# Kernel tuning notes

Hardware: AMD Instinct MI355X
Metric: run time of the kernel (lower is better)

## Reference

```python
import jax, jax.numpy as jnp
import numpy as np

N, D, NUM_CLASSES = 4096, 1024, 64


def setup_inputs() -> dict:
    key = jax.random.key(0)
    k1, k2 = jax.random.split(key)
    inputs = jax.random.normal(k1, (N, D), dtype=jnp.float32)
    labels = jax.random.randint(k2, (N,), 0, NUM_CLASSES, dtype=jnp.int64)
    return {"inputs": inputs, "labels": labels}


def reference(inputs, labels):
    # dist_mat = inputs @ inputs.T  (raw dot-product 'cosine_dist', no normalization)
    dist = jnp.matmul(inputs, inputs.T)  # [N, N]
    n = inputs.shape[0]
    same = labels[:, None] == labels[None, :]          # [N, N]
    eye = jnp.eye(n, dtype=bool)
    is_pos = same & ~eye                               # same label, excluding self
    is_neg = ~same                                     # different label
    # hardest-positive: +2 penalty on non-positive entries, then row argmin
    d_ap = jnp.where(is_pos, dist, dist + 2.0)
    # 'easiest' negative: +2 penalty on non-negative entries, then row argmin
    d_an = jnp.where(is_neg, dist, dist + 2.0)
    id_ap = jnp.argmin(d_ap, axis=1)                   # [N]
    id_an = jnp.argmin(d_an, axis=1)                   # [N]
    # (The original also computes a semi-hard id_an_semi, but returns id_an;
    #  that block is dead code w.r.t. the output, so it is omitted.)
    return (inputs[id_ap], inputs[id_an])
```

## Files before the change

kernel.cpp:

```cpp
#include <hip/hip_runtime.h>
#include <cstdint>

#define N 4096
#define D 1024
#define KC_COUNT (D / 32)
#define TB (N / 128)
#define NBLK (TB * (TB + 1) / 2)

typedef _Float16 f16;
typedef __attribute__((ext_vector_type(4))) _Float16 f16x4;
typedef __attribute__((ext_vector_type(8))) _Float16 f16x8;
typedef __attribute__((ext_vector_type(4))) float f32x4;

__device__ __forceinline__ unsigned int orderable(float f) {
    unsigned int b = __float_as_uint(f);
    return (b & 0x80000000u) ? ~b : (b | 0x80000000u);
}

#define ROW_PAD 8
#define ROW_STRIDE (D + ROW_PAD)
__global__ __launch_bounds__(256) void split_swizzle(
    const float* __restrict__ X, f16* __restrict__ Xsw,
    unsigned long long* __restrict__ keys)
{
    __shared__ f16 Hs[16 * ROW_STRIDE];
    __shared__ f16 Ls[16 * ROW_STRIDE];
    const int tid = threadIdx.x;
    const int rg = blockIdx.x;
    if (tid < 32) keys[rg * 32 + tid] = 0xFFFFFFFFFFFFFFFFull;

    const float4* src = (const float4*)(X + (size_t)rg * 16 * D);
#pragma unroll
    for (int it = 0; it < 16; ++it) {
        const int idx4 = it * 256 + tid;
        const int row = idx4 >> 8;
        const int k4 = (idx4 & 255) * 4;
        const float4 v = src[idx4];
        const float xs[4] = {v.x, v.y, v.z, v.w};
        f16x4 h, l;
#pragma unroll
        for (int i = 0; i < 4; ++i) {
            f16 hh = (f16)xs[i];
            h[i] = hh;
            l[i] = (f16)(xs[i] - (float)hh);
        }
        *(f16x4*)(Hs + row * ROW_STRIDE + k4) = h;
        *(f16x4*)(Ls + row * ROW_STRIDE + k4) = l;
    }
    __syncthreads();
#pragma unroll
    for (int hl = 0; hl < 2; ++hl) {
        const f16* lds = hl ? Ls : Hs;
#pragma unroll
        for (int it = 0; it < 8; ++it) {
            const int o = it * 256 + tid;
            const int kc = o >> 6, lo_ = o & 63;
            const int q = lo_ >> 4, m = lo_ & 15;
            const uint4 v = *(const uint4*)(lds + m * ROW_STRIDE + kc * 32 + q * 8);
            *(uint4*)(Xsw + (((size_t)rg * KC_COUNT + kc) * 2 + hl) * 512 + lo_ * 8) = v;
        }
    }
}

__global__ __launch_bounds__(256) void gemm_argmin_sym(
    const f16* __restrict__ Xsw, const int* __restrict__ labels,
    unsigned long long* __restrict__ keys_ap,
    unsigned long long* __restrict__ keys_an)
{
    int r = blockIdx.x, bi = 0;
    while (r >= TB - bi) { r -= TB - bi; ++bi; }
    const int bj = bi + r;

    const int tid = threadIdx.x;
    const int lane = tid & 63;
    const int w = tid >> 6;
    const int wr = w >> 1, wc = w & 1;
    const int rowBase = bi * 128, colBase = bj * 128;

    f32x4 acc[4][4];
#pragma unroll
    for (int mi = 0; mi < 4; ++mi)
#pragma unroll
        for (int ni = 0; ni < 4; ++ni) acc[mi][ni] = (f32x4){0.f, 0.f, 0.f, 0.f};

    const f16* baseA[4];
    const f16* baseB[4];
#pragma unroll
    for (int t2 = 0; t2 < 4; ++t2) {
        const int rgA = bi * 8 + wr * 4 + t2;
        const int rgB = bj * 8 + wc * 4 + t2;
        baseA[t2] = Xsw + ((size_t)rgA * KC_COUNT * 2) * 512 + lane * 8;
        baseB[t2] = Xsw + ((size_t)rgB * KC_COUNT * 2) * 512 + lane * 8;
    }

    f16x8 ah0[4], al0[4], bh0[4], bl0[4];
    f16x8 ah1[4], al1[4], bh1[4], bl1[4];

#define LOAD_SET(AH, AL, BH, BL, KC_) \
    _Pragma("unroll") \
    for (int t2 = 0; t2 < 4; ++t2) { \
        const f16* pa = baseA[t2] + (size_t)(KC_) * 1024; \
        const f16* pb = baseB[t2] + (size_t)(KC_) * 1024; \
        AH[t2] = *(const f16x8*)(pa); \
        AL[t2] = *(const f16x8*)(pa + 512); \
        BH[t2] = *(const f16x8*)(pb); \
        BL[t2] = *(const f16x8*)(pb + 512); \
    }

#define MFMA_SET(AH, AL, BH, BL) \
    _Pragma("unroll") \
    for (int mi = 0; mi < 4; ++mi) \
        _Pragma("unroll") \
        for (int ni = 0; ni < 4; ++ni) { \
            acc[mi][ni] = __builtin_amdgcn_mfma_f32_16x16x32_f16( \
                AH[mi], BH[ni], acc[mi][ni], 0, 0, 0); \
            acc[mi][ni] = __builtin_amdgcn_mfma_f32_16x16x32_f16( \
                AH[mi], BL[ni], acc[mi][ni], 0, 0, 0); \
            acc[mi][ni] = __builtin_amdgcn_mfma_f32_16x16x32_f16( \
                AL[mi], BH[ni], acc[mi][ni], 0, 0, 0); \
        }

    LOAD_SET(ah0, al0, bh0, bl0, 0)
    for (int kc = 0; kc < KC_COUNT; kc += 2) {
        LOAD_SET(ah1, al1, bh1, bl1, kc + 1)
        MFMA_SET(ah0, al0, bh0, bl0)
        if (kc + 2 < KC_COUNT) {
            LOAD_SET(ah0, al0, bh0, bl0, kc + 2)
        }
        MFMA_SET(ah1, al1, bh1, bl1)
    }
#undef LOAD_SET
#undef MFMA_SET

    const int g16 = lane >> 4, c16 = lane & 15;

    int ljv[4], liv[4][4];
#pragma unroll
    for (int ni = 0; ni < 4; ++ni) ljv[ni] = labels[colBase + wc * 64 + ni * 16 + c16];
#pragma unroll
    for (int mi = 0; mi < 4; ++mi)
#pragma unroll
        for (int reg = 0; reg < 4; ++reg)
            liv[mi][reg] = labels[rowBase + wr * 64 + mi * 16 + g16 * 4 + reg];

#pragma unroll
    for (int mi = 0; mi < 4; ++mi) {
#pragma unroll
        for (int reg = 0; reg < 4; ++reg) {
            const int rloc = wr * 64 + mi * 16 + g16 * 4 + reg;
            const int i = rowBase + rloc;
            const int li = liv[mi][reg];
            float bestAp = __builtin_huge_valf(); int jAp = 0;
            float bestAn = __builtin_huge_valf(); int jAn = 0;
#pragma unroll
            for (int ni = 0; ni < 4; ++ni) {
                const int jcol = colBase + wc * 64 + ni * 16 + c16;
                const float v = acc[mi][ni][reg];
                const bool same = (li == ljv[ni]);
                const float vap = (same && (i != jcol)) ? v : v + 2.0f;
                const float van = (!same) ? v : v + 2.0f;
                if (vap < bestAp) { bestAp = vap; jAp = jcol; }
                if (van < bestAn) { bestAn = van; jAn = jcol; }
            }
            unsigned long long kap =
                ((unsigned long long)orderable(bestAp) << 32) | (unsigned)jAp;
            unsigned long long kan =
                ((unsigned long long)orderable(bestAn) << 32) | (unsigned)jAn;
#pragma unroll
            for (int off = 1; off < 16; off <<= 1) {
                unsigned long long o = __shfl_xor(kap, off); kap = o < kap ? o : kap;
                o = __shfl_xor(kan, off); kan = o < kan ? o : kan;
            }
            if (c16 == 0) {
                atomicMin(&keys_ap[i], kap);
                atomicMin(&keys_an[i], kan);
            }
        }
    }

    if (bi != bj) {
#pragma unroll
        for (int ni = 0; ni < 4; ++ni) {
            const int j = colBase + wc * 64 + ni * 16 + c16;
            const int lj = ljv[ni];
            float bestAp = __builtin_huge_valf(); int iAp = 0;
            float bestAn = __builtin_huge_valf(); int iAn = 0;
#pragma unroll
            for (int mi = 0; mi < 4; ++mi)
#pragma unroll
                for (int reg = 0; reg < 4; ++reg) {
                    const int i = rowBase + wr * 64 + mi * 16 + g16 * 4 + reg;
                    const float v = acc[mi][ni][reg];
                    const bool same = (liv[mi][reg] == lj);
                    const float vap = same ? v : v + 2.0f;
                    const float van = (!same) ? v : v + 2.0f;
                    if (vap < bestAp) { bestAp = vap; iAp = i; }
                    if (van < bestAn) { bestAn = van; iAn = i; }
                }
            unsigned long long kap =
                ((unsigned long long)orderable(bestAp) << 32) | (unsigned)iAp;
            unsigned long long kan =
                ((unsigned long long)orderable(bestAn) << 32) | (unsigned)iAn;
#pragma unroll
            for (int off = 16; off < 64; off <<= 1) {
                unsigned long long o = __shfl_xor(kap, off); kap = o < kap ? o : kap;
                o = __shfl_xor(kan, off); kan = o < kan ? o : kan;
            }
            if (g16 == 0) {
                atomicMin(&keys_ap[j], kap);
                atomicMin(&keys_an[j], kan);
            }
        }
    }
}

__global__ void gather_rows(const float* __restrict__ A,
                            const unsigned long long* __restrict__ keys_ap,
                            const unsigned long long* __restrict__ keys_an,
                            float* __restrict__ out)
{
    const int row = blockIdx.x;
    const int t = threadIdx.x;
    const int ja = (int)(keys_ap[row] & 0xFFFFFFFFull);
    const int jn = (int)(keys_an[row] & 0xFFFFFFFFull);
    const float4* Av = (const float4*)A;
    float4* Ov = (float4*)out;
    Ov[(size_t)row * (D / 4) + t]       = Av[(size_t)ja * (D / 4) + t];
    Ov[(size_t)(N + row) * (D / 4) + t] = Av[(size_t)jn * (D / 4) + t];
}

extern "C" void kernel_launch(void* const* d_in, const int* in_sizes, int n_in,
                              void* d_out, int out_size, void* d_ws, size_t ws_size,
                              hipStream_t stream) {
    const float* A = (const float*)d_in[0];
    const int* labels = (const int*)d_in[1];
    float* out = (float*)d_out;

    unsigned long long* keys = (unsigned long long*)d_ws;
    f16* Xsw = (f16*)((char*)d_ws + 65536);

    split_swizzle<<<N / 16, 256, 0, stream>>>(A, Xsw, keys);
    gemm_argmin_sym<<<NBLK, 256, 0, stream>>>(Xsw, labels, keys, keys + N);
    gather_rows<<<N, 256, 0, stream>>>(A, keys, keys + N, out);
}
```

Before: 177.3 us.

## Switch symmetric GEMM to one wave per 64x64 upper-triangle tile

Replaces 256-thread blocks covering 128x128 upper-triangle tiles with single-wave blocks covering 64x64 tiles, and maps block index to tile coordinates with a sqrt-based closed form instead of a loop. This skips more of the redundant lower-triangle work (diagonal blocks shrink) and yields many more independent blocks (2080 vs 528) for better load balance across CUs. In exchange, each wave loads A and B fragments on its own, so the reuse that 128x128 tiles gave across the 2x2 waves is lost, and global/L2 traffic rises. Per-tile atomics to the keys array also double.

```diff
diff --git a/kernel.cpp b/kernel.cpp
--- a/kernel.cpp
+++ b/kernel.cpp
@@ -4,8 +4,8 @@
 #define N 4096
 #define D 1024
 #define KC_COUNT (D / 32)
-#define TB (N / 128)
-#define NBLK (TB * (TB + 1) / 2)
+#define TG (N / 64)
+#define NWAVE (TG * (TG + 1) / 2)
 
 typedef _Float16 f16;
 typedef __attribute__((ext_vector_type(4))) _Float16 f16x4;
@@ -62,20 +62,20 @@
     }
 }
 
-__global__ __launch_bounds__(256) void gemm_argmin_sym(
+__global__ __launch_bounds__(64) void gemm_argmin_sym(
     const f16* __restrict__ Xsw, const int* __restrict__ labels,
     unsigned long long* __restrict__ keys_ap,
     unsigned long long* __restrict__ keys_an)
 {
-    int r = blockIdx.x, bi = 0;
-    while (r >= TB - bi) { r -= TB - bi; ++bi; }
-    const int bj = bi + r;
-
-    const int tid = threadIdx.x;
-    const int lane = tid & 63;
-    const int w = tid >> 6;
-    const int wr = w >> 1, wc = w & 1;
-    const int rowBase = bi * 128, colBase = bj * 128;
+    int r = blockIdx.x;
+    int ti = (int)((2.0f * TG + 1.0f -
+                    sqrtf((2.0f * TG + 1.0f) * (2.0f * TG + 1.0f) - 8.0f * (float)r)) * 0.5f);
+    while (ti > 0 && r < ti * TG - ti * (ti - 1) / 2) --ti;
+    while (r >= (ti + 1) * TG - ti * (ti + 1) / 2) ++ti;
+    const int tj = ti + (r - (ti * TG - ti * (ti - 1) / 2));
+
+    const int lane = threadIdx.x & 63;
+    const int rowBase = ti * 64, colBase = tj * 64;
 
     f32x4 acc[4][4];
 #pragma unroll
@@ -87,8 +87,8 @@
     const f16* baseB[4];
 #pragma unroll
     for (int t2 = 0; t2 < 4; ++t2) {
-        const int rgA = bi * 8 + wr * 4 + t2;
-        const int rgB = bj * 8 + wc * 4 + t2;
+        const int rgA = ti * 4 + t2;
+        const int rgB = tj * 4 + t2;
         baseA[t2] = Xsw + ((size_t)rgA * KC_COUNT * 2) * 512 + lane * 8;
         baseB[t2] = Xsw + ((size_t)rgB * KC_COUNT * 2) * 512 + lane * 8;
     }
@@ -136,25 +136,24 @@
 
     int ljv[4], liv[4][4];
 #pragma unroll
-    for (int ni = 0; ni < 4; ++ni) ljv[ni] = labels[colBase + wc * 64 + ni * 16 + c16];
+    for (int ni = 0; ni < 4; ++ni) ljv[ni] = labels[colBase + ni * 16 + c16];
 #pragma unroll
     for (int mi = 0; mi < 4; ++mi)
 #pragma unroll
         for (int reg = 0; reg < 4; ++reg)
-            liv[mi][reg] = labels[rowBase + wr * 64 + mi * 16 + g16 * 4 + reg];
+            liv[mi][reg] = labels[rowBase + mi * 16 + g16 * 4 + reg];
 
 #pragma unroll
     for (int mi = 0; mi < 4; ++mi) {
 #pragma unroll
         for (int reg = 0; reg < 4; ++reg) {
-            const int rloc = wr * 64 + mi * 16 + g16 * 4 + reg;
-            const int i = rowBase + rloc;
+            const int i = rowBase + mi * 16 + g16 * 4 + reg;
             const int li = liv[mi][reg];
             float bestAp = __builtin_huge_valf(); int jAp = 0;
             float bestAn = __builtin_huge_valf(); int jAn = 0;
 #pragma unroll
             for (int ni = 0; ni < 4; ++ni) {
-                const int jcol = colBase + wc * 64 + ni * 16 + c16;
+                const int jcol = colBase + ni * 16 + c16;
                 const float v = acc[mi][ni][reg];
                 const bool same = (li == ljv[ni]);
                 const float vap = (same && (i != jcol)) ? v : v + 2.0f;
@@ -178,10 +177,10 @@
         }
     }
 
-    if (bi != bj) {
+    if (ti != tj) {
 #pragma unroll
         for (int ni = 0; ni < 4; ++ni) {
-            const int j = colBase + wc * 64 + ni * 16 + c16;
+            const int j = colBase + ni * 16 + c16;
             const int lj = ljv[ni];
             float bestAp = __builtin_huge_valf(); int iAp = 0;
             float bestAn = __builtin_huge_valf(); int iAn = 0;
@@ -189,7 +188,7 @@
             for (int mi = 0; mi < 4; ++mi)
 #pragma unroll
                 for (int reg = 0; reg < 4; ++reg) {
-                    const int i = rowBase + wr * 64 + mi * 16 + g16 * 4 + reg;
+                    const int i = rowBase + mi * 16 + g16 * 4 + reg;
                     const float v = acc[mi][ni][reg];
                     const bool same = (liv[mi][reg] == lj);
                     const float vap = same ? v : v + 2.0f;
@@ -240,6 +239,6 @@
     f16* Xsw = (f16*)((char*)d_ws + 65536);
 
     split_swizzle<<<N / 16, 256, 0, stream>>>(A, Xsw, keys);
-    gemm_argmin_sym<<<NBLK, 256, 0, stream>>>(Xsw, labels, keys, keys + N);
+    gemm_argmin_sym<<<NWAVE, 64, 0, stream>>>(Xsw, labels, keys, keys + N);
     gather_rows<<<N, 256, 0, stream>>>(A, keys, keys + N, out);
 }
```

Result: no change. 174.1 us (-1.8%).
